# Performance work log

Measured on AMD Instinct MI355X. Metric: run time of the kernel, lower is better.

The kernel has to match this reference:

```python
import jax, jax.numpy as jnp
import numpy as np

N = 50000      # nodes
E = 800000     # edges (avg degree 16)
IN = 128       # in_dim0
H = 96         # hidden_dim
BN_EPS = 1e-5
PN_SCALE = 20.0


def setup_inputs() -> dict:
    key = jax.random.key(0)
    ks = jax.random.split(key, 12)
    s_in = 1.0 / np.sqrt(IN)
    s_h = 1.0 / np.sqrt(H)
    return {
        "x": jax.random.normal(ks[0], (N, IN), jnp.float32),
        "edge_index": jax.random.randint(ks[1], (2, E), 0, N, jnp.int32),
        # mlp0: Linear(in_dim0 -> hidden)
        "W0": jax.random.uniform(ks[2], (H, IN), jnp.float32, -s_in, s_in),
        "b0": jax.random.uniform(ks[3], (H,), jnp.float32, -s_in, s_in),
        # GIN MLP layer 1: Linear(hidden -> hidden) + BatchNorm
        "W1": jax.random.uniform(ks[4], (H, H), jnp.float32, -s_h, s_h),
        "b1": jax.random.uniform(ks[5], (H,), jnp.float32, -s_h, s_h),
        "gamma": jnp.ones((H,), jnp.float32),
        "beta": jnp.zeros((H,), jnp.float32),
        # GIN MLP layer 2: Linear(hidden -> hidden)
        "W2": jax.random.uniform(ks[6], (H, H), jnp.float32, -s_h, s_h),
        "b2": jax.random.uniform(ks[7], (H,), jnp.float32, -s_h, s_h),
    }


def reference(x, edge_index, W0, b0, W1, b1, gamma, beta, W2, b2):
    # h0 = mlp0(x)
    h0 = x @ W0.T + b0                                   # [N, H]

    # GINConv (eps=0): z_i = h0_i + sum_{j->i} h0_j
    src, dst = edge_index[0], edge_index[1]
    agg = jax.ops.segment_sum(h0[src], dst, num_segments=N)  # [N, H]
    z = h0 + agg

    # GIN MLP (layer_num=2): Linear -> BatchNorm(train) -> ReLU -> Linear
    h = z @ W1.T + b1
    mean = h.mean(axis=0)
    var = h.var(axis=0)                                  # biased, like torch BN
    h = (h - mean) * jax.lax.rsqrt(var + BN_EPS) * gamma + beta
    h = jax.nn.relu(h)
    l1 = h @ W2.T + b2                                   # [N, H]

    # PairNorm 'PN-SCS', scale=20
    col_mean = l1.mean(axis=0)
    rownorm = jnp.sqrt(1e-6 + jnp.sum(l1 * l1, axis=1, keepdims=True))
    l1 = PN_SCALE * l1 / rownorm - col_mean

    return (l1, h0)
```

## Files before the change

kernel.cpp:

```cpp
#include <hip/hip_runtime.h>

#define NN 50000
#define IN_DIM 128
#define HD 96
#define BN_EPS 1e-5f
#define PN_SCALE 20.0f
#define SCAN_NB 196
#define NREP 4

using bf16x8 = __attribute__((ext_vector_type(8))) short;
using f32x4  = __attribute__((ext_vector_type(4))) float;

__device__ __forceinline__ float4 ld4(const float* p) { return *(const float4*)p; }
__device__ __forceinline__ float4 add4(float4 a, float4 b) {
    return make_float4(a.x + b.x, a.y + b.y, a.z + b.z, a.w + b.w);
}

__device__ __forceinline__ short bfr(float f) {
    unsigned u = __float_as_uint(f);
    unsigned r = u + 0x7fffu + ((u >> 16) & 1u);
    return (short)(r >> 16);
}
__device__ __forceinline__ float bf2f(unsigned short s) {
    return __uint_as_float((unsigned)s << 16);
}
__device__ __forceinline__ bf16x8 cvt8(float4 a, float4 b) {
    bf16x8 r;
    r[0] = bfr(a.x); r[1] = bfr(a.y); r[2] = bfr(a.z); r[3] = bfr(a.w);
    r[4] = bfr(b.x); r[5] = bfr(b.y); r[6] = bfr(b.z); r[7] = bfr(b.w);
    return r;
}

__global__ void zero_kernel(float* stats, int* cnt) {
    int i = blockIdx.x * blockDim.x + threadIdx.x;
    if (i < 1024) stats[i] = 0.0f;
    int j = i - 1024;
    if (j >= 0 && j < NREP * NN) cnt[j] = 0;
}

template<int K, int MODE>
__global__ __launch_bounds__(256) void gemm_mfma(
    const float* A, const float* __restrict__ W, const float* __restrict__ bias,
    float* out, unsigned short* __restrict__ out_bf,
    const float* __restrict__ scale, const float* __restrict__ shift,
    float* __restrict__ gsum, float* __restrict__ gsumsq,
    float* __restrict__ gcol, float* __restrict__ growss,
    const int* __restrict__ ei, int* __restrict__ hist_cnt, int E)
{
    constexpr int P     = K + 8;
    constexpr int NS    = K / 32;
    constexpr int KD4   = K / 4;
    constexpr int WITER = (96 * KD4) / 256;
    constexpr int WL_SH  = 96 * P;
    constexpr int WL_TOT = (20608 > WL_SH) ? 20608 : WL_SH;
    __shared__ short Wl[WL_TOT];

    const int t    = threadIdx.x;
    const int l    = t & 63;
    const int w    = t >> 6;
    const int l15  = l & 15;
    const int lh   = l >> 4;
    const int base = blockIdx.x * 64;

    const int  arow = base + w * 16 + l15;
    const bool aok  = arow < NN;
    const float* Ap = A + (size_t)arow * K + lh * 8;
    const float4 Z4 = make_float4(0.f, 0.f, 0.f, 0.f);

    float4 pa[2 * NS];
#pragma unroll
    for (int s = 0; s < NS; ++s) {
        pa[2 * s]     = aok ? ld4(Ap + s * 32)     : Z4;
        pa[2 * s + 1] = aok ? ld4(Ap + s * 32 + 4) : Z4;
    }
    float4 wv[WITER];
#pragma unroll
    for (int i = 0; i < WITER; ++i) {
        int c = t + i * 256;
        int row = c / KD4, kq = c - row * KD4;
        wv[i] = ld4(W + (size_t)row * K + kq * 4);
    }
    float4 scv[2 * NS], shv[2 * NS];
    if (MODE == 2) {
#pragma unroll
        for (int s = 0; s < 2 * NS; ++s) {
            scv[s] = ld4(scale + (s >> 1) * 32 + lh * 8 + (s & 1) * 4);
            shv[s] = ld4(shift + (s >> 1) * 32 + lh * 8 + (s & 1) * 4);
        }
    }

    if (MODE == 0) {
        int e0 = (blockIdx.x * 256 + t) * 4;
        if (e0 + 4 <= E) {
            int4 d4 = *(const int4*)(ei + E + e0);
            atomicAdd(&hist_cnt[0 * NN + d4.x], 1);
            atomicAdd(&hist_cnt[1 * NN + d4.y], 1);
            atomicAdd(&hist_cnt[2 * NN + d4.z], 1);
            atomicAdd(&hist_cnt[3 * NN + d4.w], 1);
        } else {
            for (int i = 0; i < 4; ++i) {
                int e = e0 + i;
                if (e < E) atomicAdd(&hist_cnt[(e & 3) * NN + ei[E + e]], 1);
            }
        }
    }

    bf16x8 af[NS];
#pragma unroll
    for (int s = 0; s < NS; ++s) {
        float4 q0 = pa[2 * s], q1 = pa[2 * s + 1];
        if (MODE == 2) {
            float4 sc0 = scv[2 * s], sh0 = shv[2 * s];
            float4 sc1 = scv[2 * s + 1], sh1 = shv[2 * s + 1];
            q0.x = fmaxf(q0.x * sc0.x + sh0.x, 0.f);
            q0.y = fmaxf(q0.y * sc0.y + sh0.y, 0.f);
            q0.z = fmaxf(q0.z * sc0.z + sh0.z, 0.f);
            q0.w = fmaxf(q0.w * sc0.w + sh0.w, 0.f);
            q1.x = fmaxf(q1.x * sc1.x + sh1.x, 0.f);
            q1.y = fmaxf(q1.y * sc1.y + sh1.y, 0.f);
            q1.z = fmaxf(q1.z * sc1.z + sh1.z, 0.f);
            q1.w = fmaxf(q1.w * sc1.w + sh1.w, 0.f);
        }
        af[s] = cvt8(q0, q1);
    }

#pragma unroll
    for (int i = 0; i < WITER; ++i) {
        int c = t + i * 256;
        int row = c / KD4, kq = c - row * KD4;
        short4 s4v;
        s4v.x = bfr(wv[i].x); s4v.y = bfr(wv[i].y);
        s4v.z = bfr(wv[i].z); s4v.w = bfr(wv[i].w);
        *(short4*)(Wl + row * P + kq * 4) = s4v;
    }
    __syncthreads();

    f32x4 acc[6];
#pragma unroll
    for (int n = 0; n < 6; ++n) acc[n] = (f32x4){0.f, 0.f, 0.f, 0.f};

#pragma unroll
    for (int s = 0; s < NS; ++s) {
        const short* wp = Wl + s * 32 + lh * 8;
#pragma unroll
        for (int n = 0; n < 6; ++n) {
            bf16x8 bf = *(const bf16x8*)(wp + (n * 16 + l15) * P);
            acc[n] = __builtin_amdgcn_mfma_f32_16x16x32_bf16(af[s], bf, acc[n], 0, 0, 0);
        }
    }

    float cv[6][4];
#pragma unroll
    for (int n = 0; n < 6; ++n) {
        float b = bias[n * 16 + l15];
#pragma unroll
        for (int r = 0; r < 4; ++r) cv[n][r] = acc[n][r] + b;
    }
    int crow[4]; bool cok[4];
#pragma unroll
    for (int r = 0; r < 4; ++r) {
        crow[r] = base + w * 16 + lh * 4 + r;
        cok[r]  = crow[r] < NN;
    }

    if (MODE == 0) {
        __syncthreads();
        float* Cl = (float*)Wl;
#pragma unroll
        for (int n = 0; n < 6; ++n)
#pragma unroll
            for (int r = 0; r < 4; ++r)
                Cl[(w * 16 + lh * 4 + r) * 100 + n * 16 + l15] = cv[n][r];
        __syncthreads();
        int lrow = t >> 2;
        int q4   = t & 3;
        int grow = base + lrow;
        if (grow < NN) {
            float* o = out + (size_t)grow * HD;
            unsigned short* ob = out_bf + (size_t)grow * HD;
            const float* cr = Cl + lrow * 100;
#pragma unroll
            for (int k = 0; k < 6; ++k) {
                int c4 = q4 + k * 4;
                float4 v = *(const float4*)(cr + c4 * 4);
                *(float4*)(o + c4 * 4) = v;
                ushort4 sv;
                sv.x = (unsigned short)bfr(v.x);
                sv.y = (unsigned short)bfr(v.y);
                sv.z = (unsigned short)bfr(v.z);
                sv.w = (unsigned short)bfr(v.w);
                *(ushort4*)(ob + c4 * 4) = sv;
            }
        }
    } else {
#pragma unroll
        for (int r = 0; r < 4; ++r) {
            if (cok[r]) {
                float* o = out + (size_t)crow[r] * HD + l15;
#pragma unroll
                for (int n = 0; n < 6; ++n) o[n * 16] = cv[n][r];
            }
        }
    }

    if (MODE == 1) {
        float s[6], q[6];
#pragma unroll
        for (int n = 0; n < 6; ++n) {
            s[n] = 0.f; q[n] = 0.f;
#pragma unroll
            for (int r = 0; r < 4; ++r) {
                float v = cok[r] ? cv[n][r] : 0.f;
                s[n] += v; q[n] += v * v;
            }
        }
#pragma unroll
        for (int n = 0; n < 6; ++n) {
            s[n] += __shfl_xor(s[n], 16); s[n] += __shfl_xor(s[n], 32);
            q[n] += __shfl_xor(q[n], 16); q[n] += __shfl_xor(q[n], 32);
        }
        __syncthreads();
        float* red0 = (float*)Wl;
        float* red1 = red0 + 384;
        if (lh == 0) {
#pragma unroll
            for (int n = 0; n < 6; ++n) {
                red0[w * 96 + n * 16 + l15] = s[n];
                red1[w * 96 + n * 16 + l15] = q[n];
            }
        }
        __syncthreads();
        if (t < HD) {
            float S = red0[t] + red0[96 + t] + red0[192 + t] + red0[288 + t];
            float Q = red1[t] + red1[96 + t] + red1[192 + t] + red1[288 + t];
            atomicAdd(&gsum[t], S);
            atomicAdd(&gsumsq[t], Q);
        }
    }

    if (MODE == 2) {
        float s[6];
#pragma unroll
        for (int n = 0; n < 6; ++n) {
            s[n] = 0.f;
#pragma unroll
            for (int r = 0; r < 4; ++r) s[n] += cok[r] ? cv[n][r] : 0.f;
        }
#pragma unroll
        for (int n = 0; n < 6; ++n) {
            s[n] += __shfl_xor(s[n], 16); s[n] += __shfl_xor(s[n], 32);
        }
        float rq[4];
#pragma unroll
        for (int r = 0; r < 4; ++r) {
            float v = 0.f;
#pragma unroll
            for (int n = 0; n < 6; ++n) v = fmaf(cv[n][r], cv[n][r], v);
            v += __shfl_xor(v, 1); v += __shfl_xor(v, 2);
            v += __shfl_xor(v, 4); v += __shfl_xor(v, 8);
            rq[r] = v;
        }
        __syncthreads();
        float* red0 = (float*)Wl;
        if (lh == 0) {
#pragma unroll
            for (int n = 0; n < 6; ++n) red0[w * 96 + n * 16 + l15] = s[n];
        }
        __syncthreads();
        if (t < HD) {
            float S = red0[t] + red0[96 + t] + red0[192 + t] + red0[288 + t];
            atomicAdd(&gcol[t], S);
        }
        if (l15 == 0) {
#pragma unroll
            for (int r = 0; r < 4; ++r)
                if (cok[r]) growss[crow[r]] = rq[r];
        }
    }
}

__global__ __launch_bounds__(256) void scan_part1(const int* __restrict__ cnt,
                                                  int* __restrict__ bsum) {
    __shared__ int sh[256];
    int i = blockIdx.x * 256 + threadIdx.x;
    int t = threadIdx.x;
    int v = 0;
    if (i < NN)
        v = cnt[i] + cnt[NN + i] + cnt[2 * NN + i] + cnt[3 * NN + i];
    sh[t] = v;
    __syncthreads();
    for (int off = 128; off > 0; off >>= 1) {
        if (t < off) sh[t] += sh[t + off];
        __syncthreads();
    }
    if (t == 0) bsum[blockIdx.x] = sh[0];
}

__global__ __launch_bounds__(256) void scan_part2(int* __restrict__ bsum) {
    __shared__ int sh[256];
    int t = threadIdx.x;
    int v = (t < SCAN_NB) ? bsum[t] : 0;
    sh[t] = v;
    __syncthreads();
    for (int off = 1; off < 256; off <<= 1) {
        int u = sh[t];
        if (t >= off) u += sh[t - off];
        __syncthreads();
        sh[t] = u;
        __syncthreads();
    }
    if (t < SCAN_NB) bsum[t] = sh[t] - v;
}

__global__ __launch_bounds__(256) void scan_part3(int* __restrict__ cnt,
                                                  const int* __restrict__ bsum,
                                                  int* __restrict__ rowptr) {
    __shared__ int sh[256];
    int i = blockIdx.x * 256 + threadIdx.x;
    int t = threadIdx.x;
    int v = 0;
    if (i < NN)
        v = cnt[i] + cnt[NN + i] + cnt[2 * NN + i] + cnt[3 * NN + i];
    sh[t] = v;
    __syncthreads();
    for (int off = 1; off < 256; off <<= 1) {
        int u = sh[t];
        if (t >= off) u += sh[t - off];
        __syncthreads();
        sh[t] = u;
        __syncthreads();
    }
    int excl = sh[t] - v + bsum[blockIdx.x];
    if (i < NN) { rowptr[i] = excl; cnt[i] = excl; }
    if (i == NN - 1) rowptr[NN] = excl + v;
}

__global__ __launch_bounds__(256) void fill_kernel(const int* __restrict__ ei,
                                                   int* __restrict__ cursor,
                                                   int* __restrict__ srcs, int E) {
    int t2 = blockIdx.x * 256 + threadIdx.x;
    int e0 = t2 * 2;
    int src[2], dst[2];
#pragma unroll
    for (int i = 0; i < 2; ++i) {
        int e = e0 + i;
        bool ok = e < E;
        dst[i] = ok ? ei[E + e] : -1;
        src[i] = ok ? ei[e] : 0;
    }
    for (int pass = 0; pass < 7; ++pass) {
#pragma unroll
        for (int i = 0; i < 2; ++i) {
            if (dst[i] >= 0 && (dst[i] >> 13) == pass) {
                int slot = atomicAdd(&cursor[dst[i]], 1);
                srcs[slot] = src[i];
            }
        }
    }
}

__global__ __launch_bounds__(192) void gather_kernel(
    const float* __restrict__ h0, const unsigned short* __restrict__ h0b,
    const int* __restrict__ rowptr, const int* __restrict__ srcs,
    float* __restrict__ z)
{
    const int tid = threadIdx.x;
    const int rl  = tid / 24;
    const int c   = tid - rl * 24;
    const int row = blockIdx.x * 8 + rl;
    if (row >= NN) return;

    const int p0 = rowptr[row];
    const int p1 = rowptr[row + 1];

    float4 acc = ld4(h0 + (size_t)row * HD + c * 4);

    int p = p0;
    for (; p + 8 <= p1; p += 8) {
        int s0 = srcs[p + 0], s1 = srcs[p + 1], s2 = srcs[p + 2], s3 = srcs[p + 3];
        int s4 = srcs[p + 4], s5 = srcs[p + 5], s6 = srcs[p + 6], s7 = srcs[p + 7];
        ushort4 v0 = *(const ushort4*)(h0b + (size_t)s0 * HD + c * 4);
        ushort4 v1 = *(const ushort4*)(h0b + (size_t)s1 * HD + c * 4);
        ushort4 v2 = *(const ushort4*)(h0b + (size_t)s2 * HD + c * 4);
        ushort4 v3 = *(const ushort4*)(h0b + (size_t)s3 * HD + c * 4);
        ushort4 v4 = *(const ushort4*)(h0b + (size_t)s4 * HD + c * 4);
        ushort4 v5 = *(const ushort4*)(h0b + (size_t)s5 * HD + c * 4);
        ushort4 v6 = *(const ushort4*)(h0b + (size_t)s6 * HD + c * 4);
        ushort4 v7 = *(const ushort4*)(h0b + (size_t)s7 * HD + c * 4);
        acc.x += bf2f(v0.x) + bf2f(v1.x) + bf2f(v2.x) + bf2f(v3.x)
               + bf2f(v4.x) + bf2f(v5.x) + bf2f(v6.x) + bf2f(v7.x);
        acc.y += bf2f(v0.y) + bf2f(v1.y) + bf2f(v2.y) + bf2f(v3.y)
               + bf2f(v4.y) + bf2f(v5.y) + bf2f(v6.y) + bf2f(v7.y);
        acc.z += bf2f(v0.z) + bf2f(v1.z) + bf2f(v2.z) + bf2f(v3.z)
               + bf2f(v4.z) + bf2f(v5.z) + bf2f(v6.z) + bf2f(v7.z);
        acc.w += bf2f(v0.w) + bf2f(v1.w) + bf2f(v2.w) + bf2f(v3.w)
               + bf2f(v4.w) + bf2f(v5.w) + bf2f(v6.w) + bf2f(v7.w);
    }
    for (; p < p1; ++p) {
        ushort4 v = *(const ushort4*)(h0b + (size_t)srcs[p] * HD + c * 4);
        acc.x += bf2f(v.x); acc.y += bf2f(v.y);
        acc.z += bf2f(v.z); acc.w += bf2f(v.w);
    }

    *(float4*)(z + (size_t)row * HD + c * 4) = acc;
}

__global__ void bn_finalize_kernel(const float* __restrict__ sum, const float* __restrict__ sumsq,
                                   const float* __restrict__ gamma, const float* __restrict__ beta,
                                   float* __restrict__ scale, float* __restrict__ shift)
{
    int f = threadIdx.x;
    if (f < HD) {
        float mean = sum[f] * (1.0f / NN);
        float var  = fmaxf(sumsq[f] * (1.0f / NN) - mean * mean, 0.0f);
        float rstd = rsqrtf(var + BN_EPS);
        float sc = rstd * gamma[f];
        scale[f] = sc;
        shift[f] = beta[f] - mean * sc;
    }
}

__global__ __launch_bounds__(256) void pn_kernel(float* l1, const float* __restrict__ colsum,
                                                 const float* __restrict__ rowss)
{
    int idx = blockIdx.x * 256 + threadIdx.x;
    if (idx >= NN * 24) return;
    int row = idx / 24;
    int q = idx - row * 24;
    float rs = rsqrtf(1e-6f + rowss[row]);
    float4 v = ld4(l1 + (size_t)idx * 4);
    float4 cm = ld4(colsum + q * 4);
    v.x = PN_SCALE * v.x * rs - cm.x * (1.0f / NN);
    v.y = PN_SCALE * v.y * rs - cm.y * (1.0f / NN);
    v.z = PN_SCALE * v.z * rs - cm.z * (1.0f / NN);
    v.w = PN_SCALE * v.w * rs - cm.w * (1.0f / NN);
    *(float4*)(l1 + (size_t)idx * 4) = v;
}

extern "C" void kernel_launch(void* const* d_in, const int* in_sizes, int n_in,
                              void* d_out, int out_size, void* d_ws, size_t ws_size,
                              hipStream_t stream) {
    const float* x     = (const float*)d_in[0];
    const int*   ei    = (const int*)d_in[1];
    const float* W0    = (const float*)d_in[2];
    const float* b0    = (const float*)d_in[3];
    const float* W1    = (const float*)d_in[4];
    const float* b1    = (const float*)d_in[5];
    const float* gamma = (const float*)d_in[6];
    const float* beta  = (const float*)d_in[7];
    const float* W2    = (const float*)d_in[8];
    const float* b2    = (const float*)d_in[9];

    float* out_l1 = (float*)d_out;
    float* out_h0 = out_l1 + (size_t)NN * HD;

    float* stats   = (float*)d_ws;
    float* s_sum   = stats;
    float* s_sumsq = stats + HD;
    float* s_col   = stats + 2 * HD;
    float* s_scale = stats + 288;
    float* s_shift = stats + 384;
    float* rowss = stats + 1024;
    int* cnt    = (int*)(rowss + NN);
    int* rowptr = cnt + NREP * NN;
    int* bsum   = rowptr + NN + 2;
    int* srcs   = bsum + 256;
    unsigned short* h0b =
        (unsigned short*)(((uintptr_t)(srcs + 800000) + 15) & ~(uintptr_t)15);

    const int E = in_sizes[1] / 2;
    const int GB = (NN + 63) / 64;

    zero_kernel<<<(1024 + NREP * NN + 255) / 256, 256, 0, stream>>>(stats, cnt);
    gemm_mfma<IN_DIM, 0><<<GB, 256, 0, stream>>>(x, W0, b0, out_h0, h0b,
                                                 nullptr, nullptr,
                                                 nullptr, nullptr, nullptr, nullptr,
                                                 ei, cnt, E);
    scan_part1<<<SCAN_NB, 256, 0, stream>>>(cnt, bsum);
    scan_part2<<<1, 256, 0, stream>>>(bsum);
    scan_part3<<<SCAN_NB, 256, 0, stream>>>(cnt, bsum, rowptr);
    fill_kernel<<<(E / 2 + 255) / 256, 256, 0, stream>>>(ei, cnt, srcs, E);
    gather_kernel<<<(NN + 7) / 8, 192, 0, stream>>>(out_h0, h0b, rowptr, srcs, out_l1);
    gemm_mfma<HD, 1><<<GB, 256, 0, stream>>>(out_l1, W1, b1, out_l1, nullptr,
                                             nullptr, nullptr,
                                             s_sum, s_sumsq, nullptr, nullptr,
                                             nullptr, nullptr, 0);
    bn_finalize_kernel<<<1, 128, 0, stream>>>(s_sum, s_sumsq, gamma, beta, s_scale, s_shift);
    gemm_mfma<HD, 2><<<GB, 256, 0, stream>>>(out_l1, W2, b2, out_l1, nullptr,
                                             s_scale, s_shift,
                                             nullptr, nullptr, s_col, rowss,
                                             nullptr, nullptr, 0);
    pn_kernel<<<(NN * 24 + 255) / 256, 256, 0, stream>>>(out_l1, s_col, rowss);
}
```

Baseline: 287.0 us.

## Fuse CSR neighbor gather into the first GIN MLP GEMM

Removes the standalone gather kernel and performs the neighbor aggregation inside gemm_mfma MODE 1. Each lane loads bf16 neighbor rows directly into its A-fragment accumulators, adding them to the h0 row it already loaded, before converting to bf16 for the MFMA. This avoids writing z to global memory and reading it back, and saves a launch. In exchange, the gather runs with the GEMM's 16-rows-per-wave thread mapping, which may give less parallelism and worse latency hiding for irregular degrees.

```diff
diff --git a/kernel.cpp b/kernel.cpp
--- a/kernel.cpp
+++ b/kernel.cpp
@@ -12,9 +12,6 @@
 using f32x4  = __attribute__((ext_vector_type(4))) float;
 
 __device__ __forceinline__ float4 ld4(const float* p) { return *(const float4*)p; }
-__device__ __forceinline__ float4 add4(float4 a, float4 b) {
-    return make_float4(a.x + b.x, a.y + b.y, a.z + b.z, a.w + b.w);
-}
 
 __device__ __forceinline__ short bfr(float f) {
     unsigned u = __float_as_uint(f);
@@ -45,7 +42,9 @@
     const float* __restrict__ scale, const float* __restrict__ shift,
     float* __restrict__ gsum, float* __restrict__ gsumsq,
     float* __restrict__ gcol, float* __restrict__ growss,
-    const int* __restrict__ ei, int* __restrict__ hist_cnt, int E)
+    const int* __restrict__ ei, int* __restrict__ hist_cnt, int E,
+    const unsigned short* __restrict__ g_h0b, const int* __restrict__ g_rowptr,
+    const int* __restrict__ g_srcs)
 {
     constexpr int P     = K + 8;
     constexpr int NS    = K / 32;
@@ -101,6 +100,58 @@
             for (int i = 0; i < 4; ++i) {
                 int e = e0 + i;
                 if (e < E) atomicAdd(&hist_cnt[(e & 3) * NN + ei[E + e]], 1);
+            }
+        }
+    }
+
+    if (MODE == 1) {
+        int p0v = 0, p1v = 0;
+        if (aok) { p0v = g_rowptr[arow]; p1v = g_rowptr[arow + 1]; }
+        int p = p0v;
+        for (; p + 4 <= p1v; p += 4) {
+            int s0 = g_srcs[p], s1 = g_srcs[p + 1];
+            int s2 = g_srcs[p + 2], s3 = g_srcs[p + 3];
+            bf16x8 n0[NS], n1[NS], n2[NS], n3[NS];
+#pragma unroll
+            for (int s = 0; s < NS; ++s) {
+                n0[s] = *(const bf16x8*)(g_h0b + (size_t)s0 * HD + s * 32 + lh * 8);
+                n1[s] = *(const bf16x8*)(g_h0b + (size_t)s1 * HD + s * 32 + lh * 8);
+                n2[s] = *(const bf16x8*)(g_h0b + (size_t)s2 * HD + s * 32 + lh * 8);
+                n3[s] = *(const bf16x8*)(g_h0b + (size_t)s3 * HD + s * 32 + lh * 8);
+            }
+#pragma unroll
+            for (int s = 0; s < NS; ++s) {
+                pa[2*s].x   += bf2f((unsigned short)n0[s][0]) + bf2f((unsigned short)n1[s][0])
+                             + bf2f((unsigned short)n2[s][0]) + bf2f((unsigned short)n3[s][0]);
+                pa[2*s].y   += bf2f((unsigned short)n0[s][1]) + bf2f((unsigned short)n1[s][1])
+                             + bf2f((unsigned short)n2[s][1]) + bf2f((unsigned short)n3[s][1]);
+                pa[2*s].z   += bf2f((unsigned short)n0[s][2]) + bf2f((unsigned short)n1[s][2])
+                             + bf2f((unsigned short)n2[s][2]) + bf2f((unsigned short)n3[s][2]);
+                pa[2*s].w   += bf2f((unsigned short)n0[s][3]) + bf2f((unsigned short)n1[s][3])
+                             + bf2f((unsigned short)n2[s][3]) + bf2f((unsigned short)n3[s][3]);
+                pa[2*s+1].x += bf2f((unsigned short)n0[s][4]) + bf2f((unsigned short)n1[s][4])
+                             + bf2f((unsigned short)n2[s][4]) + bf2f((unsigned short)n3[s][4]);
+                pa[2*s+1].y += bf2f((unsigned short)n0[s][5]) + bf2f((unsigned short)n1[s][5])
+                             + bf2f((unsigned short)n2[s][5]) + bf2f((unsigned short)n3[s][5]);
+                pa[2*s+1].z += bf2f((unsigned short)n0[s][6]) + bf2f((unsigned short)n1[s][6])
+                             + bf2f((unsigned short)n2[s][6]) + bf2f((unsigned short)n3[s][6]);
+                pa[2*s+1].w += bf2f((unsigned short)n0[s][7]) + bf2f((unsigned short)n1[s][7])
+                             + bf2f((unsigned short)n2[s][7]) + bf2f((unsigned short)n3[s][7]);
+            }
+        }
+        for (; p < p1v; ++p) {
+            int s0 = g_srcs[p];
+#pragma unroll
+            for (int s = 0; s < NS; ++s) {
+                bf16x8 v = *(const bf16x8*)(g_h0b + (size_t)s0 * HD + s * 32 + lh * 8);
+                pa[2*s].x   += bf2f((unsigned short)v[0]);
+                pa[2*s].y   += bf2f((unsigned short)v[1]);
+                pa[2*s].z   += bf2f((unsigned short)v[2]);
+                pa[2*s].w   += bf2f((unsigned short)v[3]);
+                pa[2*s+1].x += bf2f((unsigned short)v[4]);
+                pa[2*s+1].y += bf2f((unsigned short)v[5]);
+                pa[2*s+1].z += bf2f((unsigned short)v[6]);
+                pa[2*s+1].w += bf2f((unsigned short)v[7]);
             }
         }
     }
@@ -357,52 +408,6 @@
             }
         }
     }
-}
-
-__global__ __launch_bounds__(192) void gather_kernel(
-    const float* __restrict__ h0, const unsigned short* __restrict__ h0b,
-    const int* __restrict__ rowptr, const int* __restrict__ srcs,
-    float* __restrict__ z)
-{
-    const int tid = threadIdx.x;
-    const int rl  = tid / 24;
-    const int c   = tid - rl * 24;
-    const int row = blockIdx.x * 8 + rl;
-    if (row >= NN) return;
-
-    const int p0 = rowptr[row];
-    const int p1 = rowptr[row + 1];
-
-    float4 acc = ld4(h0 + (size_t)row * HD + c * 4);
-
-    int p = p0;
-    for (; p + 8 <= p1; p += 8) {
-        int s0 = srcs[p + 0], s1 = srcs[p + 1], s2 = srcs[p + 2], s3 = srcs[p + 3];
-        int s4 = srcs[p + 4], s5 = srcs[p + 5], s6 = srcs[p + 6], s7 = srcs[p + 7];
-        ushort4 v0 = *(const ushort4*)(h0b + (size_t)s0 * HD + c * 4);
-        ushort4 v1 = *(const ushort4*)(h0b + (size_t)s1 * HD + c * 4);
-        ushort4 v2 = *(const ushort4*)(h0b + (size_t)s2 * HD + c * 4);
-        ushort4 v3 = *(const ushort4*)(h0b + (size_t)s3 * HD + c * 4);
-        ushort4 v4 = *(const ushort4*)(h0b + (size_t)s4 * HD + c * 4);
-        ushort4 v5 = *(const ushort4*)(h0b + (size_t)s5 * HD + c * 4);
-        ushort4 v6 = *(const ushort4*)(h0b + (size_t)s6 * HD + c * 4);
-        ushort4 v7 = *(const ushort4*)(h0b + (size_t)s7 * HD + c * 4);
-        acc.x += bf2f(v0.x) + bf2f(v1.x) + bf2f(v2.x) + bf2f(v3.x)
-               + bf2f(v4.x) + bf2f(v5.x) + bf2f(v6.x) + bf2f(v7.x);
-        acc.y += bf2f(v0.y) + bf2f(v1.y) + bf2f(v2.y) + bf2f(v3.y)
-               + bf2f(v4.y) + bf2f(v5.y) + bf2f(v6.y) + bf2f(v7.y);
-        acc.z += bf2f(v0.z) + bf2f(v1.z) + bf2f(v2.z) + bf2f(v3.z)
-               + bf2f(v4.z) + bf2f(v5.z) + bf2f(v6.z) + bf2f(v7.z);
-        acc.w += bf2f(v0.w) + bf2f(v1.w) + bf2f(v2.w) + bf2f(v3.w)
-               + bf2f(v4.w) + bf2f(v5.w) + bf2f(v6.w) + bf2f(v7.w);
-    }
-    for (; p < p1; ++p) {
-        ushort4 v = *(const ushort4*)(h0b + (size_t)srcs[p] * HD + c * 4);
-        acc.x += bf2f(v.x); acc.y += bf2f(v.y);
-        acc.z += bf2f(v.z); acc.w += bf2f(v.w);
-    }
-
-    *(float4*)(z + (size_t)row * HD + c * 4) = acc;
 }
 
 __global__ void bn_finalize_kernel(const float* __restrict__ sum, const float* __restrict__ sumsq,
@@ -475,20 +480,22 @@
     gemm_mfma<IN_DIM, 0><<<GB, 256, 0, stream>>>(x, W0, b0, out_h0, h0b,
                                                  nullptr, nullptr,
                                                  nullptr, nullptr, nullptr, nullptr,
-                                                 ei, cnt, E);
+                                                 ei, cnt, E,
+                                                 nullptr, nullptr, nullptr);
     scan_part1<<<SCAN_NB, 256, 0, stream>>>(cnt, bsum);
     scan_part2<<<1, 256, 0, stream>>>(bsum);
     scan_part3<<<SCAN_NB, 256, 0, stream>>>(cnt, bsum, rowptr);
     fill_kernel<<<(E / 2 + 255) / 256, 256, 0, stream>>>(ei, cnt, srcs, E);
-    gather_kernel<<<(NN + 7) / 8, 192, 0, stream>>>(out_h0, h0b, rowptr, srcs, out_l1);
-    gemm_mfma<HD, 1><<<GB, 256, 0, stream>>>(out_l1, W1, b1, out_l1, nullptr,
+    gemm_mfma<HD, 1><<<GB, 256, 0, stream>>>(out_h0, W1, b1, out_l1, nullptr,
                                              nullptr, nullptr,
                                              s_sum, s_sumsq, nullptr, nullptr,
-                                             nullptr, nullptr, 0);
+                                             nullptr, nullptr, 0,
+                                             h0b, rowptr, srcs);
     bn_finalize_kernel<<<1, 128, 0, stream>>>(s_sum, s_sumsq, gamma, beta, s_scale, s_shift);
     gemm_mfma<HD, 2><<<GB, 256, 0, stream>>>(out_l1, W2, b2, out_l1, nullptr,
                                              s_scale, s_shift,
                                              nullptr, nullptr, s_col, rowss,
-                                             nullptr, nullptr, 0);
+                                             nullptr, nullptr, 0,
+                                             nullptr, nullptr, nullptr);
     pn_kernel<<<(NN * 24 + 255) / 256, 256, 0, stream>>>(out_l1, s_col, rowss);
 }
```

Result: no change. 282.1 us (-1.7%).
